# Performance work log

Measured on AMD Instinct MI355X. Metric: run time of the kernel, lower is better.

## Reference

```python
import jax, jax.numpy as jnp
import numpy as np


def setup_inputs() -> dict:
    key = jax.random.key(0)
    k1, k2, k3, k4 = jax.random.split(key, 4)
    N, E, DIN, H1, H2 = 100000, 1600000, 128, 64, 32
    x = jax.random.normal(k1, (N, DIN), dtype=jnp.float32)
    edge_index = jax.random.randint(k2, (2, E), 0, N, dtype=jnp.int64)
    # Glorot-style scaled init for the two GCN weight matrices (no bias)
    W1 = jax.random.normal(k3, (DIN, H1), dtype=jnp.float32) * (1.0 / np.sqrt(DIN))
    W2 = jax.random.normal(k4, (H1, H2), dtype=jnp.float32) * (1.0 / np.sqrt(H1))
    return {"x": x, "edge_index": edge_index, "W1": W1, "W2": W2}


def reference(x, edge_index, W1, W2):
    N = x.shape[0]
    loop = jnp.arange(N, dtype=edge_index.dtype)
    src = jnp.concatenate([edge_index[0], loop])  # [E+N]
    dst = jnp.concatenate([edge_index[1], loop])  # [E+N]
    # symmetric GCN normalization with self-loops (edge_weight = 1)
    deg = jax.ops.segment_sum(jnp.ones(src.shape, x.dtype), dst, num_segments=N)
    dinv = jnp.where(deg > 0, jax.lax.rsqrt(deg), 0.0)
    norm = dinv[src] * dinv[dst]  # [E+N]

    def gcn_conv(h, W):
        h = h @ W  # transform first (PyG GCNConv order)
        msg = h[src] * norm[:, None]  # gather + scale
        return jax.ops.segment_sum(msg, dst, num_segments=N)  # scatter-add

    hidden1 = jax.nn.relu(gcn_conv(x, W1))
    z = gcn_conv(hidden1, W2)
    return z
```

## Files before the change

kernel.cpp:

```cpp
#include <hip/hip_runtime.h>
#include <hip/hip_fp16.h>

#define DIN 128
#define H1  64
#define H2  32
#define NCH 256
#define BSH 8

typedef _Float16 f16x8 __attribute__((ext_vector_type(8)));
typedef _Float16 f16x4 __attribute__((ext_vector_type(4)));
typedef float    f32x4 __attribute__((ext_vector_type(4)));

__global__ __launch_bounds__(256) void k_hist(const int* __restrict__ dst,
        int* __restrict__ H, int E, int NB, int chunk) {
    __shared__ int lh[512];
    int c = blockIdx.x, tid = threadIdx.x;
    for (int b = tid; b < NB; b += 256) lh[b] = 0;
    __syncthreads();
    int e0 = c * chunk, e1 = min(E, e0 + chunk);
    for (int e = e0 + tid; e < e1; e += 256)
        atomicAdd(&lh[dst[e] >> BSH], 1);
    __syncthreads();
    for (int b = tid; b < NB; b += 256) H[(size_t)b * NCH + c] = lh[b];
}

__global__ __launch_bounds__(256) void k_scan1(const int* __restrict__ in,
        int* __restrict__ out, int* __restrict__ partial, int N) {
    int tid = threadIdx.x;
    int base = blockIdx.x * 1024 + tid * 4;
    int v0 = (base + 0 < N) ? in[base + 0] : 0;
    int v1 = (base + 1 < N) ? in[base + 1] : 0;
    int v2 = (base + 2 < N) ? in[base + 2] : 0;
    int v3 = (base + 3 < N) ? in[base + 3] : 0;
    int sum = v0 + v1 + v2 + v3;
    int lane = tid & 63, wid = tid >> 6;
    int x = sum;
#pragma unroll
    for (int off = 1; off < 64; off <<= 1) {
        int y = __shfl_up(x, off, 64);
        if (lane >= off) x += y;
    }
    __shared__ int wsum[4];
    if (lane == 63) wsum[wid] = x;
    __syncthreads();
    int wbase = 0;
    for (int w = 0; w < wid; ++w) wbase += wsum[w];
    int excl = wbase + x - sum;
    if (base + 0 < N) out[base + 0] = excl;
    if (base + 1 < N) out[base + 1] = excl + v0;
    if (base + 2 < N) out[base + 2] = excl + v0 + v1;
    if (base + 3 < N) out[base + 3] = excl + v0 + v1 + v2;
    if (tid == 0) partial[blockIdx.x] = wsum[0] + wsum[1] + wsum[2] + wsum[3];
}

__global__ __launch_bounds__(256) void k_scan2(int* __restrict__ partial, int nb) {
    int tid = threadIdx.x;
    int v = (tid < nb) ? partial[tid] : 0;
    __shared__ int tmp[256];
    tmp[tid] = v;
    __syncthreads();
    for (int off = 1; off < 256; off <<= 1) {
        int y = (tid >= off) ? tmp[tid - off] : 0;
        __syncthreads();
        tmp[tid] += y;
        __syncthreads();
    }
    if (tid < nb) partial[tid] = tmp[tid] - v;
}

__global__ __launch_bounds__(256) void k_bsort(const int* __restrict__ src,
        const int* __restrict__ dst, const int* __restrict__ H,
        const int* __restrict__ partial, int* __restrict__ ep,
        int E, int NB, int chunk) {
    __shared__ int cur[512];
    int c = blockIdx.x, tid = threadIdx.x;
    for (int b = tid; b < NB; b += 256) {
        int idx = b * NCH + c;
        cur[b] = H[idx] + partial[idx >> 10];
    }
    __syncthreads();
    int e0 = c * chunk, e1 = min(E, e0 + chunk);
    for (int e = e0 + tid; e < e1; e += 256) {
        int s = src[e], d = dst[e];
        int pos = atomicAdd(&cur[d >> BSH], 1);
        ep[pos] = s | ((d & ((1 << BSH) - 1)) << 20);
    }
}

__global__ __launch_bounds__(256) void k_csr(const int* __restrict__ ep,
        const int* __restrict__ H, const int* __restrict__ partial,
        int* __restrict__ degi, int* __restrict__ rowptr, float* __restrict__ dinv,
        int* __restrict__ csr_src, int E, int N, int NB) {
    __shared__ int cnt[256], pos[256], wsum[4];
    int b = blockIdx.x, tid = threadIdx.x;
    cnt[tid] = 0;
    int i0 = b * NCH;
    int bstart = H[i0] + partial[i0 >> 10];
    int bend = E;
    if (b + 1 < NB) {
        int i1 = (b + 1) * NCH;
        bend = H[i1] + partial[i1 >> 10];
    }
    int base8 = (bstart + b * 2048 + 7) & ~7;
    __syncthreads();
    for (int e = bstart + tid; e < bend; e += 256)
        atomicAdd(&cnt[ep[e] >> 20], 1);
    __syncthreads();
    int v = cnt[tid];
    int n = (b << BSH) + tid;
    int d8 = (n < N) ? ((v + 7) & ~7) : 0;
    int lane = tid & 63, wid = tid >> 6;
    int x = d8;
#pragma unroll
    for (int off = 1; off < 64; off <<= 1) {
        int y = __shfl_up(x, off, 64);
        if (lane >= off) x += y;
    }
    if (lane == 63) wsum[wid] = x;
    __syncthreads();
    int wbase = 0;
    for (int w = 0; w < wid; ++w) wbase += wsum[w];
    int startv = base8 + wbase + x - d8;
    if (n < N) {
        degi[n]   = v;
        dinv[n]   = rsqrtf((float)v + 1.0f);
        rowptr[n] = startv;
    }
    pos[tid] = startv;
    __syncthreads();
    for (int e = bstart + tid; e < bend; e += 256) {
        int p = ep[e];
        int q = atomicAdd(&pos[p >> 20], 1);
        csr_src[q] = p & 0xFFFFF;
    }
    __syncthreads();
    if (n < N) {
        int d = degi[n], dd8 = (d + 7) & ~7;
        for (int z = startv + d; z < startv + dd8; ++z)
            csr_src[z] = N;
    }
}

__global__ __launch_bounds__(256) void k_mgemm1(const float* __restrict__ x,
        const float* __restrict__ W1, const float* __restrict__ dinv,
        _Float16* __restrict__ t1h, int N) {
    __shared__ _Float16 sA[64 * 128];
    __shared__ _Float16 sB[64 * 128];
    int tid = threadIdx.x;
    int row0 = blockIdx.x * 64;
    if (blockIdx.x == 0 && tid < 8)
        ((f32x4*)(t1h + (size_t)N * H1))[tid] = (f32x4){0.f, 0.f, 0.f, 0.f};
#pragma unroll
    for (int i = 0; i < 8; ++i) {
        int idx4 = tid + 256 * i;
        int r = idx4 >> 5, c4 = idx4 & 31;
        int row = row0 + r;
        float4 v = make_float4(0.f, 0.f, 0.f, 0.f);
        if (row < N) v = *(const float4*)&x[(size_t)row * DIN + c4 * 4];
        f16x4 h;
        h[0] = (_Float16)v.x; h[1] = (_Float16)v.y;
        h[2] = (_Float16)v.z; h[3] = (_Float16)v.w;
        int byte = (c4 * 8) ^ ((r & 7) << 4);
        *(f16x4*)((char*)sA + r * 256 + byte) = h;
    }
    {
        int n = tid & 63, kq = tid >> 6;
        _Float16 tmp[32];
#pragma unroll
        for (int kk = 0; kk < 32; ++kk)
            tmp[kk] = (_Float16)W1[(size_t)(kq * 32 + kk) * H1 + n];
#pragma unroll
        for (int j = 0; j < 4; ++j) {
            int byte = ((kq * 32 + j * 8) * 2) ^ ((n & 7) << 4);
            *(f16x8*)((char*)sB + n * 256 + byte) = *(f16x8*)&tmp[j * 8];
        }
    }
    __syncthreads();
    int lane = tid & 63, w = tid >> 6;
    int lr = lane & 15, kg = lane >> 4;
    f32x4 acc[4] = {};
    int ar = w * 16 + lr;
    const char* pa = (const char*)sA + ar * 256;
    int axor = (ar & 7) << 4;
#pragma unroll
    for (int ks = 0; ks < 4; ++ks) {
        int kb = ks * 64 + kg * 16;
        f16x8 a = *(const f16x8*)(pa + (kb ^ axor));
#pragma unroll
        for (int nt = 0; nt < 4; ++nt) {
            int bn = nt * 16 + lr;
            f16x8 b = *(const f16x8*)((const char*)sB + bn * 256 + (kb ^ ((bn & 7) << 4)));
            acc[nt] = __builtin_amdgcn_mfma_f32_16x16x32_f16(a, b, acc[nt], 0, 0, 0);
        }
    }
#pragma unroll
    for (int rg = 0; rg < 4; ++rg) {
        int R = row0 + w * 16 + kg * 4 + rg;
        if (R < N) {
            float dv = dinv[R];
#pragma unroll
            for (int nt = 0; nt < 4; ++nt)
                t1h[(size_t)R * H1 + nt * 16 + lr] = (_Float16)(acc[nt][rg] * dv);
        }
    }
}

__global__ __launch_bounds__(256) void k_mgemm2(const _Float16* __restrict__ aggh,
        const float* __restrict__ W2, const float* __restrict__ dinv,
        _Float16* __restrict__ t2h, int N) {
    __shared__ _Float16 sA[64 * 64];
    __shared__ _Float16 sB[32 * 64];
    int tid = threadIdx.x;
    int row0 = blockIdx.x * 64;
    if (blockIdx.x == 0 && tid < 4)
        ((f32x4*)(t2h + (size_t)N * H2))[tid] = (f32x4){0.f, 0.f, 0.f, 0.f};
#pragma unroll
    for (int i = 0; i < 2; ++i) {
        int idx8 = tid + 256 * i;
        int r = idx8 >> 3, c8 = idx8 & 7;
        int row = row0 + r;
        f16x8 h = {};
        if (row < N) h = *(const f16x8*)&aggh[(size_t)row * H1 + c8 * 8];
        int byte = (c8 * 16) ^ ((r & 7) << 4);
        *(f16x8*)((char*)sA + r * 128 + byte) = h;
    }
    {
        int n = tid & 31, kq = tid >> 5;
        _Float16 tmp[8];
#pragma unroll
        for (int kk = 0; kk < 8; ++kk)
            tmp[kk] = (_Float16)W2[(size_t)(kq * 8 + kk) * H2 + n];
        int byte = (kq * 16) ^ ((n & 7) << 4);
        *(f16x8*)((char*)sB + n * 128 + byte) = *(f16x8*)&tmp[0];
    }
    __syncthreads();
    int lane = tid & 63, w = tid >> 6;
    int lr = lane & 15, kg = lane >> 4;
    f32x4 acc[2] = {};
    int ar = w * 16 + lr;
    const char* pa = (const char*)sA + ar * 128;
    int axor = (ar & 7) << 4;
#pragma unroll
    for (int ks = 0; ks < 2; ++ks) {
        int kb = ks * 64 + kg * 16;
        f16x8 a = *(const f16x8*)(pa + (kb ^ axor));
#pragma unroll
        for (int nt = 0; nt < 2; ++nt) {
            int bn = nt * 16 + lr;
            f16x8 b = *(const f16x8*)((const char*)sB + bn * 128 + (kb ^ ((bn & 7) << 4)));
            acc[nt] = __builtin_amdgcn_mfma_f32_16x16x32_f16(a, b, acc[nt], 0, 0, 0);
        }
    }
#pragma unroll
    for (int rg = 0; rg < 4; ++rg) {
        int R = row0 + w * 16 + kg * 4 + rg;
        if (R < N) {
            float dv = dinv[R];
#pragma unroll
            for (int nt = 0; nt < 2; ++nt)
                t2h[(size_t)R * H2 + nt * 16 + lr] = (_Float16)(acc[nt][rg] * dv);
        }
    }
}

template <int LOGL, bool FUSE>
__global__ __launch_bounds__(256) void k_aggq(const int* __restrict__ rowptr,
        const int* __restrict__ degi, const int* __restrict__ csr_src,
        const float* __restrict__ dinv, const _Float16* __restrict__ tp,
        void* __restrict__ outv, int N) {
    const int L = 1 << LOGL;
    const int F = L * 8;
    int local = threadIdx.x >> LOGL;
    int j = threadIdx.x & (L - 1);
    int n = blockIdx.x * (256 >> LOGL) + local;
    if (n >= N) return;
    int start = rowptr[n];
    int deg = degi[n];
    f16x8 sv = *(const f16x8*)&tp[(size_t)n * F + j * 8];
    float acc[8];
#pragma unroll
    for (int t = 0; t < 8; ++t) acc[t] = (float)sv[t];
    for (int k = 0; k < deg; k += 8) {
        int4 ra = *(const int4*)&csr_src[start + k];
        int4 rb = *(const int4*)&csr_src[start + k + 4];
        int idx[8] = {ra.x, ra.y, ra.z, ra.w, rb.x, rb.y, rb.z, rb.w};
        f16x8 g[8];
#pragma unroll
        for (int u = 0; u < 8; ++u)
            g[u] = *(const f16x8*)&tp[(size_t)idx[u] * F + j * 8];
#pragma unroll
        for (int u = 0; u < 8; ++u)
#pragma unroll
            for (int t = 0; t < 8; ++t)
                acc[t] += (float)g[u][t];
    }
    float dv = dinv[n];
    if (FUSE) {
        f16x8 o;
#pragma unroll
        for (int t = 0; t < 8; ++t) o[t] = (_Float16)fmaxf(acc[t] * dv, 0.f);
        *(f16x8*)((_Float16*)outv + (size_t)n * F + j * 8) = o;
    } else {
        float* op = (float*)outv + (size_t)n * F + j * 8;
        f32x4 o0 = {acc[0] * dv, acc[1] * dv, acc[2] * dv, acc[3] * dv};
        f32x4 o1 = {acc[4] * dv, acc[5] * dv, acc[6] * dv, acc[7] * dv};
        *(f32x4*)op = o0;
        *(f32x4*)(op + 4) = o1;
    }
}

extern "C" void kernel_launch(void* const* d_in, const int* in_sizes, int n_in,
                              void* d_out, int out_size, void* d_ws, size_t ws_size,
                              hipStream_t stream) {
    const float* x  = (const float*)d_in[0];
    const int*   ei = (const int*)d_in[1];
    const float* W1 = (const float*)d_in[2];
    const float* W2 = (const float*)d_in[3];

    const int N = in_sizes[0] / DIN;
    const int E = in_sizes[1] / 2;
    const int* src = ei;
    const int* dst = ei + E;

    const int NB    = (N + (1 << BSH) - 1) >> BSH;
    const int NBNCH = NB * NCH;
    const int chunk = (E + NCH - 1) / NCH;

    float*    dinv    = (float*)d_ws;
    int*      degi    = (int*)(dinv + N);
    int*      rowptr  = degi + N;
    int*      H       = rowptr + N;
    int*      partial = H + NBNCH;
    int*      csr_src = partial + 256;
    _Float16* t1h     = (_Float16*)(csr_src + E + 2048 * NB + 8);
    _Float16* agg1h   = t1h + (size_t)(N + 1) * H1;
    _Float16* t2h     = t1h;
    float*    out     = (float*)d_out;
    int*      ep      = (int*)t1h;

    k_hist<<<NCH, 256, 0, stream>>>(dst, H, E, NB, chunk);
    k_scan1<<<(NBNCH + 1023) / 1024, 256, 0, stream>>>(H, H, partial, NBNCH);
    k_scan2<<<1, 256, 0, stream>>>(partial, (NBNCH + 1023) / 1024);
    k_bsort<<<NCH, 256, 0, stream>>>(src, dst, H, partial, ep, E, NB, chunk);
    k_csr<<<NB, 256, 0, stream>>>(ep, H, partial, degi, rowptr, dinv, csr_src, E, N, NB);

    const int ntile = (N + 63) / 64;

    k_mgemm1<<<ntile, 256, 0, stream>>>(x, W1, dinv, t1h, N);
    k_aggq<3, true><<<(N + 31) / 32, 256, 0, stream>>>(rowptr, degi, csr_src, dinv,
                                                       t1h, agg1h, N);

    k_mgemm2<<<ntile, 256, 0, stream>>>(agg1h, W2, dinv, t2h, N);
    k_aggq<2, false><<<(N + 63) / 64, 256, 0, stream>>>(rowptr, degi, csr_src, dinv,
                                                        t2h, out, N);
}
```

Baseline: 145.3 us.

## Double-buffer neighbor gathers in aggregation and widen edge-sort chunking

The aggregation kernel now prefetches the next batch of eight neighbor rows into a second register buffer while accumulating the current batch. This is meant to hide gather latency behind the arithmetic. The bucket-sort passes now use twice as many chunks (512 instead of 256) to spread histogram and scatter work over more blocks. A small extra kernel folds the scan partial sums into the histogram up front, so the bsort and csr kernels read final offsets directly. The trade-offs are higher register pressure in the aggregation kernel, one more kernel launch, and a larger histogram.

Result: no change. 147.7 us (+1.7%).

```diff
diff --git a/kernel.cpp b/kernel.cpp
--- a/kernel.cpp
+++ b/kernel.cpp
@@ -4,7 +4,7 @@
 #define DIN 128
 #define H1  64
 #define H2  32
-#define NCH 256
+#define NCH 512
 #define BSH 8
 
 typedef _Float16 f16x8 __attribute__((ext_vector_type(8)));
@@ -68,16 +68,17 @@
     if (tid < nb) partial[tid] = tmp[tid] - v;
 }
 
+__global__ void k_scan3b(int* __restrict__ a, const int* __restrict__ partial, int n) {
+    int i = blockIdx.x * blockDim.x + threadIdx.x;
+    if (i < n) a[i] += partial[i >> 10];
+}
+
 __global__ __launch_bounds__(256) void k_bsort(const int* __restrict__ src,
         const int* __restrict__ dst, const int* __restrict__ H,
-        const int* __restrict__ partial, int* __restrict__ ep,
-        int E, int NB, int chunk) {
+        int* __restrict__ ep, int E, int NB, int chunk) {
     __shared__ int cur[512];
     int c = blockIdx.x, tid = threadIdx.x;
-    for (int b = tid; b < NB; b += 256) {
-        int idx = b * NCH + c;
-        cur[b] = H[idx] + partial[idx >> 10];
-    }
+    for (int b = tid; b < NB; b += 256) cur[b] = H[(size_t)b * NCH + c];
     __syncthreads();
     int e0 = c * chunk, e1 = min(E, e0 + chunk);
     for (int e = e0 + tid; e < e1; e += 256) {
@@ -88,19 +89,13 @@
 }
 
 __global__ __launch_bounds__(256) void k_csr(const int* __restrict__ ep,
-        const int* __restrict__ H, const int* __restrict__ partial,
-        int* __restrict__ degi, int* __restrict__ rowptr, float* __restrict__ dinv,
-        int* __restrict__ csr_src, int E, int N, int NB) {
+        const int* __restrict__ H, int* __restrict__ degi, int* __restrict__ rowptr,
+        float* __restrict__ dinv, int* __restrict__ csr_src, int E, int N, int NB) {
     __shared__ int cnt[256], pos[256], wsum[4];
     int b = blockIdx.x, tid = threadIdx.x;
     cnt[tid] = 0;
-    int i0 = b * NCH;
-    int bstart = H[i0] + partial[i0 >> 10];
-    int bend = E;
-    if (b + 1 < NB) {
-        int i1 = (b + 1) * NCH;
-        bend = H[i1] + partial[i1 >> 10];
-    }
+    int bstart = H[(size_t)b * NCH];
+    int bend = (b + 1 < NB) ? H[(size_t)(b + 1) * NCH] : E;
     int base8 = (bstart + b * 2048 + 7) & ~7;
     __syncthreads();
     for (int e = bstart + tid; e < bend; e += 256)
@@ -280,20 +275,43 @@
     float acc[8];
 #pragma unroll
     for (int t = 0; t < 8; ++t) acc[t] = (float)sv[t];
-    for (int k = 0; k < deg; k += 8) {
-        int4 ra = *(const int4*)&csr_src[start + k];
-        int4 rb = *(const int4*)&csr_src[start + k + 4];
+
+    auto load_batch = [&](f16x8* g, int off) {
+        int4 ra = *(const int4*)&csr_src[off];
+        int4 rb = *(const int4*)&csr_src[off + 4];
         int idx[8] = {ra.x, ra.y, ra.z, ra.w, rb.x, rb.y, rb.z, rb.w};
-        f16x8 g[8];
 #pragma unroll
         for (int u = 0; u < 8; ++u)
             g[u] = *(const f16x8*)&tp[(size_t)idx[u] * F + j * 8];
+    };
+    auto acc_batch = [&](const f16x8* g) {
 #pragma unroll
         for (int u = 0; u < 8; ++u)
 #pragma unroll
             for (int t = 0; t < 8; ++t)
                 acc[t] += (float)g[u][t];
-    }
+    };
+
+    int nb = (deg + 7) >> 3;
+    if (nb > 0) {
+        f16x8 A[8], B[8];
+        load_batch(A, start);
+        int kb = 1;
+        for (; kb + 1 < nb; kb += 2) {
+            load_batch(B, start + kb * 8);
+            acc_batch(A);
+            load_batch(A, start + (kb + 1) * 8);
+            acc_batch(B);
+        }
+        if (kb < nb) {
+            load_batch(B, start + kb * 8);
+            acc_batch(A);
+            acc_batch(B);
+        } else {
+            acc_batch(A);
+        }
+    }
+
     float dv = dinv[n];
     if (FUSE) {
         f16x8 o;
@@ -341,8 +359,9 @@
     k_hist<<<NCH, 256, 0, stream>>>(dst, H, E, NB, chunk);
     k_scan1<<<(NBNCH + 1023) / 1024, 256, 0, stream>>>(H, H, partial, NBNCH);
     k_scan2<<<1, 256, 0, stream>>>(partial, (NBNCH + 1023) / 1024);
-    k_bsort<<<NCH, 256, 0, stream>>>(src, dst, H, partial, ep, E, NB, chunk);
-    k_csr<<<NB, 256, 0, stream>>>(ep, H, partial, degi, rowptr, dinv, csr_src, E, N, NB);
+    k_scan3b<<<(NBNCH + 255) / 256, 256, 0, stream>>>(H, partial, NBNCH);
+    k_bsort<<<NCH, 256, 0, stream>>>(src, dst, H, ep, E, NB, chunk);
+    k_csr<<<NB, 256, 0, stream>>>(ep, H, degi, rowptr, dinv, csr_src, E, N, NB);
 
     const int ntile = (N + 63) / 64;
 
```
